# Kernel optimization log

Measured on AMD Instinct MI355X. Metric: run time of the kernel, lower is better.

## Reference

```python
import jax, jax.numpy as jnp
import numpy as np

B, SQ, C = 8, 4096, 1280
CAD = 2048
H, D = 20, 64          # heads x head_dim = hidden_size
NT = 4                 # num IP tokens
TXT = 77               # text tokens
IP_SCALE = 1.0


def setup_inputs() -> dict:
    key = jax.random.key(0)
    ks = jax.random.split(key, 9)
    s = 0.02
    return {
        "hidden_states": jax.random.normal(ks[0], (B, SQ, C), jnp.float32),
        "encoder_hidden_states": jax.random.normal(ks[1], (B, TXT + NT, CAD), jnp.float32),
        "Wq": jax.random.normal(ks[2], (C, C), jnp.float32) * s,
        "Wk": jax.random.normal(ks[3], (CAD, C), jnp.float32) * s,
        "Wv": jax.random.normal(ks[4], (CAD, C), jnp.float32) * s,
        "Wk_ip": jax.random.normal(ks[5], (CAD, C), jnp.float32) * s,
        "Wv_ip": jax.random.normal(ks[6], (CAD, C), jnp.float32) * s,
        "Wo": jax.random.normal(ks[7], (C, C), jnp.float32) * s,
        "bo": jnp.zeros((C,), jnp.float32),
    }


def _heads(x):
    # [b, s, C] -> [b, H, s, D]
    b, s, _ = x.shape
    return x.reshape(b, s, H, D).transpose(0, 2, 1, 3)


def _attend(q, k, v):
    scale = jnp.asarray(1.0 / np.sqrt(D), q.dtype)
    probs = jax.nn.softmax(jnp.einsum('bhqd,bhkd->bhqk', q, k) * scale, axis=-1)
    return jnp.einsum('bhqk,bhkd->bhqd', probs, v)


def reference(hidden_states, encoder_hidden_states, Wq, Wk, Wv, Wk_ip, Wv_ip, Wo, bo):
    residual = hidden_states
    txt = encoder_hidden_states[:, :-NT, :]   # [B, 77, CAD]
    ip = encoder_hidden_states[:, -NT:, :]    # [B, 4, CAD]

    q = _heads(hidden_states @ Wq)            # [B, H, SQ, D]
    k = _heads(txt @ Wk)
    v = _heads(txt @ Wv)
    out = _attend(q, k, v)                    # text branch

    ip_k = _heads(ip @ Wk_ip)
    ip_v = _heads(ip @ Wv_ip)
    out = out + IP_SCALE * _attend(q, ip_k, ip_v)  # IP-adapter branch

    b = out.shape[0]
    out = out.transpose(0, 2, 1, 3).reshape(b, SQ, C)  # merge heads
    out = out @ Wo + bo
    return out + residual
```

## Files before the change

### kernel.cpp

```cpp
#include <hip/hip_runtime.h>
#include <hip/hip_bf16.h>
#include <cstdint>
#include <cstddef>


typedef __bf16 bf16_t;
typedef __bf16 bf16x8 __attribute__((ext_vector_type(8)));
typedef __bf16 bf16x4 __attribute__((ext_vector_type(4)));
typedef float  f32x4  __attribute__((ext_vector_type(4)));
typedef unsigned int u32x4 __attribute__((ext_vector_type(4)));

using as3_void  = __attribute__((address_space(3))) void;
using as1_cvoid = const __attribute__((address_space(1))) void;

#define TXT_ 77

__device__ __forceinline__ bf16x8 ld16(const void* p) {
  u32x4 v = *(const u32x4*)p;
  return __builtin_bit_cast(bf16x8, v);
}

template <int EPI>
__device__ __forceinline__ void gemm256_body(
    char* smem, const bf16_t* __restrict__ A, const bf16_t* __restrict__ Bt,
    void* __restrict__ Cout, int g, int ntn, int N, int K,
    const float* __restrict__ bias, const bf16_t* __restrict__ residual)
{
  const int tid = threadIdx.x, lane = tid & 63, wid = tid >> 6;
  const int wm = wid >> 2, wn = wid & 3;

  const long bm = (long)(g / ntn) * 256;
  const long bn = (long)(g % ntn) * 256;
  const int NTk = K >> 5;

  const int srow = lane >> 2;
  const int scol = ((lane & 3) ^ ((lane >> 3) & 3)) * 8;

  auto stageA = [&](int t) {
    const int buf = t & 3;
    const long k0 = (long)t << 5;
#pragma unroll
    for (int j = 0; j < 2; ++j) {
      const int ci = j * 8 + wid;
      const bf16_t* gp = A + (bm + ci * 16 + srow) * (long)K + k0 + scol;
      __builtin_amdgcn_global_load_lds((as1_cvoid*)gp,
          (as3_void*)(smem + buf * 16384 + ci * 1024), 16, 0, 0);
    }
  };
  auto stageB = [&](int t) {
    const int buf = t & 3;
    const long k0 = (long)t << 5;
#pragma unroll
    for (int j = 0; j < 2; ++j) {
      const int ci = j * 8 + wid;
      const bf16_t* gp = Bt + (bn + ci * 16 + srow) * (long)K + k0 + scol;
      __builtin_amdgcn_global_load_lds((as1_cvoid*)gp,
          (as3_void*)(smem + 65536 + buf * 16384 + ci * 1024), 16, 0, 0);
    }
  };

  const int l15 = lane & 15, kq = lane >> 4;
  const int rc16 = (kq ^ ((l15 >> 1) & 3)) << 4;

  f32x4 acc[8][4] = {};
  bf16x8 afr[4], bfr[4];

  stageA(0); stageB(0); stageA(1); stageB(1);
  asm volatile("s_waitcnt vmcnt(4)" ::: "memory");
  __builtin_amdgcn_s_barrier();

  for (int t = 0; t < NTk; ++t) {
    const char* sa = smem + (t & 3) * 16384;
    const char* sb = smem + 65536 + (t & 3) * 16384;
    const bool pf = (t + 2 < NTk);

#pragma unroll
    for (int n = 0; n < 4; ++n)
      bfr[n] = ld16(sb + (wn * 64 + n * 16 + l15) * 64 + rc16);
#pragma unroll
    for (int m = 0; m < 4; ++m)
      afr[m] = ld16(sa + (wm * 128 + m * 16 + l15) * 64 + rc16);
    if (pf) stageA(t + 2);
    __builtin_amdgcn_s_setprio(1);
#pragma unroll
    for (int m = 0; m < 4; ++m)
#pragma unroll
      for (int n = 0; n < 4; ++n)
        acc[m][n] = __builtin_amdgcn_mfma_f32_16x16x32_bf16(afr[m], bfr[n], acc[m][n], 0, 0, 0);
    __builtin_amdgcn_s_setprio(0);

#pragma unroll
    for (int m = 0; m < 4; ++m)
      afr[m] = ld16(sa + (wm * 128 + (m + 4) * 16 + l15) * 64 + rc16);
    if (pf) stageB(t + 2);
    __builtin_amdgcn_s_setprio(1);
#pragma unroll
    for (int m = 0; m < 4; ++m)
#pragma unroll
      for (int n = 0; n < 4; ++n)
        acc[m + 4][n] = __builtin_amdgcn_mfma_f32_16x16x32_bf16(afr[m], bfr[n], acc[m + 4][n], 0, 0, 0);
    __builtin_amdgcn_s_setprio(0);

    if (t == NTk - 2) asm volatile("s_waitcnt vmcnt(0)" ::: "memory");
    else              asm volatile("s_waitcnt vmcnt(4)" ::: "memory");
    __builtin_amdgcn_s_barrier();
  }

  const int orow0 = (lane >> 4) << 2;
  if constexpr (EPI == 0) {
    bf16_t* cl = (bf16_t*)smem;
    const int lrow0 = wm * 128 + orow0;
    const int lcol0 = wn * 64 + l15;
#pragma unroll
    for (int m = 0; m < 8; ++m)
#pragma unroll
      for (int n = 0; n < 4; ++n)
#pragma unroll
        for (int r = 0; r < 4; ++r)
          cl[(lrow0 + m * 16 + r) * 256 + lcol0 + n * 16] = (bf16_t)acc[m][n][r];
    __syncthreads();
    const int rr = tid >> 5, cc = tid & 31;
#pragma unroll
    for (int s = 0; s < 16; ++s) {
      const int row = s * 16 + rr;
      const u32x4 v = *(const u32x4*)(cl + row * 256 + cc * 8);
      *(u32x4*)((bf16_t*)Cout + (bm + row) * (long)N + bn + cc * 8) = v;
    }
  } else {
#pragma unroll
    for (int m = 0; m < 8; ++m) {
#pragma unroll
      for (int n = 0; n < 4; ++n) {
        const long col = bn + wn * 64 + n * 16 + l15;
#pragma unroll
        for (int r = 0; r < 4; ++r) {
          const long row = bm + wm * 128 + m * 16 + orow0 + r;
          ((float*)Cout)[row * N + col] =
              acc[m][n][r] + bias[col] + (float)residual[row * N + col];
        }
      }
    }
  }
}

__global__ __launch_bounds__(512, 2)
void gemm1_fused(const bf16_t* __restrict__ hsb, const bf16_t* __restrict__ Wq_t,
                 bf16_t* __restrict__ qb,
                 const bf16_t* __restrict__ a_txt, const bf16_t* __restrict__ Wkv_t,
                 bf16_t* __restrict__ kv_txt,
                 const bf16_t* __restrict__ a_ip, const bf16_t* __restrict__ Wip_t,
                 bf16_t* __restrict__ kv_ip)
{
  __shared__ __align__(16) char smem[131072];
  const int bid = blockIdx.x;
  const bf16_t *A, *Bt;
  bf16_t* C;
  int g, ntn, N, K;
  if (bid < 640) {
    g = (bid & 7) * 80 + (bid >> 3);
    A = hsb; Bt = Wq_t; C = qb; ntn = 5; N = 1280; K = 1280;
  } else if (bid < 670) {
    g = bid - 640; A = a_txt; Bt = Wkv_t; C = kv_txt; ntn = 10; N = 2560; K = 2048;
  } else {
    g = bid - 670; A = a_ip; Bt = Wip_t; C = kv_ip; ntn = 10; N = 2560; K = 2048;
  }
  gemm256_body<0>(smem, A, Bt, C, g, ntn, N, K, nullptr, nullptr);
}

__global__ __launch_bounds__(512, 2)
void gemm2(const bf16_t* __restrict__ A, const bf16_t* __restrict__ Bt,
           float* __restrict__ Cout, const float* __restrict__ bias,
           const bf16_t* __restrict__ residual)
{
  __shared__ __align__(16) char smem[131072];
  const int bid = blockIdx.x;
  const int g = (bid & 7) * 80 + (bid >> 3);
  gemm256_body<2>(smem, A, Bt, Cout, g, 5, 1280, 1280, bias, residual);
}

__global__ __launch_bounds__(256, 3)
void attn_fused(const bf16_t* __restrict__ q, const bf16_t* __restrict__ kvt,
                const bf16_t* __restrict__ kvip, bf16_t* __restrict__ outp)
{
  __shared__ __align__(16) bf16_t K_lds[80 * 64];
  __shared__ __align__(16) bf16_t Kip_lds[16 * 64];
  __shared__ __align__(16) bf16_t Vt_lds[64 * 128];
  __shared__ __align__(16) bf16_t P_lds[4][16 * 128];

  const int tid = threadIdx.x, lane = tid & 63, wid = tid >> 6;
  const int h = blockIdx.y, b = blockIdx.z;
  const int kvcol = h << 6;

  for (int idx = tid; idx < 640; idx += 256) {
    const int j = idx >> 3, c = idx & 7;
    bf16x8 v = {};
    if (j < TXT_) v = ld16(kvt + (long)(b * 80 + j) * 2560 + kvcol + c * 8);
    *(bf16x8*)((char*)K_lds + j * 128 + ((c ^ (j & 7)) << 4)) = v;
  }
  if (tid < 128) {
    const int j = tid >> 3, c = tid & 7;
    bf16x8 v = {};
    if (j < 4) v = ld16(kvip + (long)(b * 4 + j) * 2560 + kvcol + c * 8);
    *(bf16x8*)((char*)Kip_lds + j * 128 + ((c ^ (j & 7)) << 4)) = v;
  }
  for (int idx = tid; idx < 1024; idx += 256) {
    const int key = idx >> 3, c = idx & 7;
    bf16x8 v = {};
    if (key < TXT_)
      v = ld16(kvt + (long)(b * 80 + key) * 2560 + 1280 + kvcol + c * 8);
    else if (key >= 96 && key < 100)
      v = ld16(kvip + (long)(b * 4 + key - 96) * 2560 + 1280 + kvcol + c * 8);
#pragma unroll
    for (int e = 0; e < 8; ++e) {
      const int d = c * 8 + e;
      *(bf16_t*)((char*)Vt_lds + d * 256 + ((key * 2) ^ ((d & 7) << 4))) = v[e];
    }
  }
  for (int idx = tid; idx < 1024; idx += 256)
    *(bf16x8*)((char*)P_lds + idx * 16) = (bf16x8){};
  __syncthreads();

  const int l15 = lane & 15, hi = lane >> 4;
  const int dblk = hi << 3;
  const int prow0 = hi << 2;
  const float scale = 0.125f;
  char* const pw = (char*)P_lds[wid];

  const long qrow0 = (long)b * 4096 + ((long)blockIdx.x << 8) + (wid << 6);
  bf16x8 qf[4][2];
#pragma unroll
  for (int ms = 0; ms < 4; ++ms) {
    const bf16_t* qp = q + (qrow0 + ms * 16 + l15) * 1280 + kvcol;
    qf[ms][0] = ld16(qp + dblk);
    qf[ms][1] = ld16(qp + 32 + dblk);
  }

#pragma unroll
  for (int ms = 0; ms < 4; ++ms) {
    f32x4 sc[5];
#pragma unroll
    for (int t = 0; t < 5; ++t) {
      const int j = (t << 4) + l15;
      const bf16x8 k0 = ld16((char*)K_lds + j * 128 + ((hi ^ (j & 7)) << 4));
      const bf16x8 k1 = ld16((char*)K_lds + j * 128 + (((4 + hi) ^ (j & 7)) << 4));
      f32x4 z = {0.f, 0.f, 0.f, 0.f};
      z = __builtin_amdgcn_mfma_f32_16x16x32_bf16(qf[ms][0], k0, z, 0, 0, 0);
      z = __builtin_amdgcn_mfma_f32_16x16x32_bf16(qf[ms][1], k1, z, 0, 0, 0);
      sc[t] = z;
    }
#pragma unroll
    for (int t = 0; t < 5; ++t) {
      const bool valid = ((t << 4) + l15) < TXT_;
#pragma unroll
      for (int r = 0; r < 4; ++r)
        sc[t][r] = valid ? sc[t][r] * scale : -1e30f;
    }

#pragma unroll
    for (int r = 0; r < 4; ++r) {
      float m = sc[0][r];
#pragma unroll
      for (int t = 1; t < 5; ++t) m = fmaxf(m, sc[t][r]);
      m = fmaxf(m, __shfl_xor(m, 1));
      m = fmaxf(m, __shfl_xor(m, 2));
      m = fmaxf(m, __shfl_xor(m, 4));
      m = fmaxf(m, __shfl_xor(m, 8));
      float l = 0.f;
#pragma unroll
      for (int t = 0; t < 5; ++t) { const float p = __expf(sc[t][r] - m); sc[t][r] = p; l += p; }
      l += __shfl_xor(l, 1);
      l += __shfl_xor(l, 2);
      l += __shfl_xor(l, 4);
      l += __shfl_xor(l, 8);
      const float inv = 1.f / l;
      const int row = prow0 + r;
#pragma unroll
      for (int t = 0; t < 5; ++t)
        *(bf16_t*)(pw + row * 256 + ((((t << 4) + l15) * 2) ^ ((row & 7) << 4))) =
            (bf16_t)(sc[t][r] * inv);
    }

    {
      const bf16x8 ki0 = ld16((char*)Kip_lds + l15 * 128 + ((hi ^ (l15 & 7)) << 4));
      const bf16x8 ki1 = ld16((char*)Kip_lds + l15 * 128 + (((4 + hi) ^ (l15 & 7)) << 4));
      f32x4 z = {0.f, 0.f, 0.f, 0.f};
      z = __builtin_amdgcn_mfma_f32_16x16x32_bf16(qf[ms][0], ki0, z, 0, 0, 0);
      z = __builtin_amdgcn_mfma_f32_16x16x32_bf16(qf[ms][1], ki1, z, 0, 0, 0);
      const bool vip = l15 < 4;
#pragma unroll
      for (int r = 0; r < 4; ++r) {
        const float s = vip ? z[r] * scale : -1e30f;
        float m = s;
        m = fmaxf(m, __shfl_xor(m, 1));
        m = fmaxf(m, __shfl_xor(m, 2));
        m = fmaxf(m, __shfl_xor(m, 4));
        m = fmaxf(m, __shfl_xor(m, 8));
        const float p = __expf(s - m);
        float l = p;
        l += __shfl_xor(l, 1);
        l += __shfl_xor(l, 2);
        l += __shfl_xor(l, 4);
        l += __shfl_xor(l, 8);
        const int row = prow0 + r;
        *(bf16_t*)(pw + row * 256 + (((96 + l15) * 2) ^ ((row & 7) << 4))) =
            (bf16_t)(p * (1.f / l));
      }
    }

    f32x4 o[4] = {};
#pragma unroll
    for (int s = 0; s < 4; ++s) {
      const bf16x8 pa =
          ld16(pw + l15 * 256 + ((((s << 2) + hi) << 4) ^ ((l15 & 7) << 4)));
#pragma unroll
      for (int n = 0; n < 4; ++n) {
        const int d = (n << 4) + l15;
        const bf16x8 vb =
            ld16((char*)Vt_lds + d * 256 + ((((s << 2) + hi) << 4) ^ ((d & 7) << 4)));
        o[n] = __builtin_amdgcn_mfma_f32_16x16x32_bf16(pa, vb, o[n], 0, 0, 0);
      }
    }

    const long orow = qrow0 + ms * 16 + prow0;
#pragma unroll
    for (int n = 0; n < 4; ++n)
#pragma unroll
      for (int r = 0; r < 4; ++r)
        outp[(orow + r) * 1280 + kvcol + (n << 4) + l15] = (bf16_t)o[n][r];
  }
}

__global__ __launch_bounds__(256)
void prep(const float* __restrict__ hs, bf16_t* __restrict__ hsb,
          const float* __restrict__ Wq, const float* __restrict__ Wo,
          const float* __restrict__ Wk, const float* __restrict__ Wv,
          const float* __restrict__ Wki, const float* __restrict__ Wvi,
          bf16_t* __restrict__ Wq_t, bf16_t* __restrict__ Wo_t,
          bf16_t* __restrict__ Wkv_t, bf16_t* __restrict__ Wip_t,
          const float* __restrict__ enc, bf16_t* __restrict__ a_txt,
          bf16_t* __restrict__ a_ip)
{
  __shared__ float tile[32][33];
  const int bid = blockIdx.x, tid = threadIdx.x;

  if (bid < 40960) {
    const long i = ((long)bid * 256 + tid) * 4;
    const float4 v = *(const float4*)(hs + i);
    bf16x4 r;
    r[0] = (bf16_t)v.x; r[1] = (bf16_t)v.y; r[2] = (bf16_t)v.z; r[3] = (bf16_t)v.w;
    *(bf16x4*)(hsb + i) = r;
  } else if (bid < 56320) {
    const int idx = bid - 40960;
    const int z = idx / 2560, rem = idx % 2560;
    const int kx = rem & 63, ny = rem >> 6;
    const float* in;
    bf16_t* out;
    int K;
    switch (z) {
      case 0:  in = Wq;  out = Wq_t;                      K = 1280; break;
      case 1:  in = Wo;  out = Wo_t;                      K = 1280; break;
      case 2:  in = Wk;  out = Wkv_t;                     K = 2048; break;
      case 3:  in = Wv;  out = Wkv_t + (long)1280 * 2048; K = 2048; break;
      case 4:  in = Wki; out = Wip_t;                     K = 2048; break;
      default: in = Wvi; out = Wip_t + (long)1280 * 2048; K = 2048; break;
    }
    const int k0 = kx * 32, n0 = ny * 32;
    if (k0 < K) {
      const int tx = tid & 31, ty = tid >> 5;
      for (int i = ty; i < 32; i += 8)
        tile[i][tx] = in[(long)(k0 + i) * 1280 + n0 + tx];
      __syncthreads();
      for (int i = ty; i < 32; i += 8)
        out[(long)(n0 + i) * K + k0 + tx] = (bf16_t)tile[tx][i];
    }
  } else {
    const long t4 = ((long)(bid - 56320) * 256 + tid) * 4;
    const long NTXT = 768L * 2048;
    bf16x4 r;
    r[0] = r[1] = r[2] = r[3] = (bf16_t)0.f;
    if (t4 < NTXT) {
      const int row = (int)(t4 >> 11), col = (int)(t4 & 2047);
      if (row < 640) {
        const int b = row / 80, j = row - b * 80;
        if (j < TXT_) {
          const float4 v = *(const float4*)(enc + (((long)(b * 81 + j)) << 11) + col);
          r[0] = (bf16_t)v.x; r[1] = (bf16_t)v.y; r[2] = (bf16_t)v.z; r[3] = (bf16_t)v.w;
        }
      }
      *(bf16x4*)(a_txt + t4) = r;
    } else {
      const long u = t4 - NTXT;
      const int row = (int)(u >> 11), col = (int)(u & 2047);
      if (row < 32) {
        const int b = row >> 2, j = row & 3;
        const float4 v = *(const float4*)(enc + (((long)(b * 81 + TXT_ + j)) << 11) + col);
        r[0] = (bf16_t)v.x; r[1] = (bf16_t)v.y; r[2] = (bf16_t)v.z; r[3] = (bf16_t)v.w;
      }
      *(bf16x4*)(a_ip + u) = r;
    }
  }
}

extern "C" void kernel_launch(void* const* d_in, const int* in_sizes, int n_in,
                              void* d_out, int out_size, void* d_ws, size_t ws_size,
                              hipStream_t stream)
{
  (void)in_sizes; (void)n_in; (void)out_size; (void)ws_size;
  const float* hs  = (const float*)d_in[0];
  const float* enc = (const float*)d_in[1];
  const float* Wq  = (const float*)d_in[2];
  const float* Wk  = (const float*)d_in[3];
  const float* Wv  = (const float*)d_in[4];
  const float* Wki = (const float*)d_in[5];
  const float* Wvi = (const float*)d_in[6];
  const float* Wo  = (const float*)d_in[7];
  const float* bo  = (const float*)d_in[8];

  char* ws = (char*)d_ws;
  size_t off = 0;
  auto alloc = [&](size_t bytes) {
    char* p = ws + off;
    off += (bytes + 255) & ~(size_t)255;
    return p;
  };
  bf16_t* buf1   = (bf16_t*)alloc(83886080);
  bf16_t* qb     = (bf16_t*)alloc(83886080);
  bf16_t* Wq_t   = (bf16_t*)alloc(3276800);
  bf16_t* Wo_t   = (bf16_t*)alloc(3276800);
  bf16_t* Wkv_t  = (bf16_t*)alloc(10485760);
  bf16_t* Wip_t  = (bf16_t*)alloc(10485760);
  bf16_t* a_txt  = (bf16_t*)alloc(3145728);
  bf16_t* a_ip   = (bf16_t*)alloc(1048576);
  bf16_t* kv_txt = (bf16_t*)alloc(3932160);
  bf16_t* kv_ip  = (bf16_t*)alloc(1310720);

  prep<<<58368, 256, 0, stream>>>(hs, buf1, Wq, Wo, Wk, Wv, Wki, Wvi,
                                  Wq_t, Wo_t, Wkv_t, Wip_t, enc, a_txt, a_ip);

  gemm1_fused<<<680, 512, 0, stream>>>(buf1, Wq_t, qb,
                                       a_txt, Wkv_t, kv_txt,
                                       a_ip, Wip_t, kv_ip);

  attn_fused<<<dim3(16, 20, 8), 256, 0, stream>>>(qb, kv_txt, kv_ip, qb);

  gemm2<<<640, 512, 0, stream>>>(qb, Wo_t, (float*)d_out, bo, buf1);
}
```

Baseline: 421.9 us.

## Load GEMM B fragments directly to registers, halve LDS footprint

The B operand is no longer staged through LDS. Each wave loads its B fragments straight from global memory into registers, double-buffered two k-steps ahead, and the loop is unrolled by two to alternate between the buffers. This halves shared memory to 64KB, so the bf16 epilogue is split into two halves to fit the staging buffer. It removes LDS traffic and LDS capacity pressure for B, at the cost of redundant global/L2 reads of B across waves and more registers.

```diff
diff --git a/kernel.cpp b/kernel.cpp
--- a/kernel.cpp
+++ b/kernel.cpp
@@ -47,36 +47,31 @@
           (as3_void*)(smem + buf * 16384 + ci * 1024), 16, 0, 0);
     }
   };
-  auto stageB = [&](int t) {
-    const int buf = t & 3;
-    const long k0 = (long)t << 5;
-#pragma unroll
-    for (int j = 0; j < 2; ++j) {
-      const int ci = j * 8 + wid;
-      const bf16_t* gp = Bt + (bn + ci * 16 + srow) * (long)K + k0 + scol;
-      __builtin_amdgcn_global_load_lds((as1_cvoid*)gp,
-          (as3_void*)(smem + 65536 + buf * 16384 + ci * 1024), 16, 0, 0);
-    }
-  };
 
   const int l15 = lane & 15, kq = lane >> 4;
   const int rc16 = (kq ^ ((l15 >> 1) & 3)) << 4;
 
+  const bf16_t* bbase = Bt + (bn + wn * 64 + l15) * (long)K + kq * 8;
+
+  auto loadB = [&](int t, bf16x8 (&bq)[4]) {
+    const long k0 = (long)t << 5;
+#pragma unroll
+    for (int n = 0; n < 4; ++n)
+      bq[n] = ld16(bbase + (long)n * 16 * K + k0);
+  };
+
   f32x4 acc[8][4] = {};
-  bf16x8 afr[4], bfr[4];
-
-  stageA(0); stageB(0); stageA(1); stageB(1);
+  bf16x8 bA[4], bB[4];
+
+  stageA(0); stageA(1);
+  loadB(0, bA); loadB(1, bB);
   asm volatile("s_waitcnt vmcnt(4)" ::: "memory");
   __builtin_amdgcn_s_barrier();
 
-  for (int t = 0; t < NTk; ++t) {
+  auto iter = [&](int t, bf16x8 (&bcur)[4]) {
     const char* sa = smem + (t & 3) * 16384;
-    const char* sb = smem + 65536 + (t & 3) * 16384;
     const bool pf = (t + 2 < NTk);
-
-#pragma unroll
-    for (int n = 0; n < 4; ++n)
-      bfr[n] = ld16(sb + (wn * 64 + n * 16 + l15) * 64 + rc16);
+    bf16x8 afr[4];
 #pragma unroll
     for (int m = 0; m < 4; ++m)
       afr[m] = ld16(sa + (wm * 128 + m * 16 + l15) * 64 + rc16);
@@ -86,45 +81,53 @@
     for (int m = 0; m < 4; ++m)
 #pragma unroll
       for (int n = 0; n < 4; ++n)
-        acc[m][n] = __builtin_amdgcn_mfma_f32_16x16x32_bf16(afr[m], bfr[n], acc[m][n], 0, 0, 0);
+        acc[m][n] = __builtin_amdgcn_mfma_f32_16x16x32_bf16(afr[m], bcur[n], acc[m][n], 0, 0, 0);
     __builtin_amdgcn_s_setprio(0);
-
 #pragma unroll
     for (int m = 0; m < 4; ++m)
       afr[m] = ld16(sa + (wm * 128 + (m + 4) * 16 + l15) * 64 + rc16);
-    if (pf) stageB(t + 2);
     __builtin_amdgcn_s_setprio(1);
 #pragma unroll
     for (int m = 0; m < 4; ++m)
 #pragma unroll
       for (int n = 0; n < 4; ++n)
-        acc[m + 4][n] = __builtin_amdgcn_mfma_f32_16x16x32_bf16(afr[m], bfr[n], acc[m + 4][n], 0, 0, 0);
+        acc[m + 4][n] = __builtin_amdgcn_mfma_f32_16x16x32_bf16(afr[m], bcur[n], acc[m + 4][n], 0, 0, 0);
     __builtin_amdgcn_s_setprio(0);
-
-    if (t == NTk - 2) asm volatile("s_waitcnt vmcnt(0)" ::: "memory");
-    else              asm volatile("s_waitcnt vmcnt(4)" ::: "memory");
+    if (pf) loadB(t + 2, bcur);
+    if (t == NTk - 2)      asm volatile("s_waitcnt vmcnt(0)" ::: "memory");
+    else if (t < NTk - 1)  asm volatile("s_waitcnt vmcnt(6)" ::: "memory");
     __builtin_amdgcn_s_barrier();
+  };
+
+  for (int t = 0; t < NTk; t += 2) {
+    iter(t, bA);
+    iter(t + 1, bB);
   }
 
   const int orow0 = (lane >> 4) << 2;
   if constexpr (EPI == 0) {
     bf16_t* cl = (bf16_t*)smem;
-    const int lrow0 = wm * 128 + orow0;
-    const int lcol0 = wn * 64 + l15;
-#pragma unroll
-    for (int m = 0; m < 8; ++m)
-#pragma unroll
-      for (int n = 0; n < 4; ++n)
-#pragma unroll
-        for (int r = 0; r < 4; ++r)
-          cl[(lrow0 + m * 16 + r) * 256 + lcol0 + n * 16] = (bf16_t)acc[m][n][r];
-    __syncthreads();
     const int rr = tid >> 5, cc = tid & 31;
 #pragma unroll
-    for (int s = 0; s < 16; ++s) {
-      const int row = s * 16 + rr;
-      const u32x4 v = *(const u32x4*)(cl + row * 256 + cc * 8);
-      *(u32x4*)((bf16_t*)Cout + (bm + row) * (long)N + bn + cc * 8) = v;
+    for (int h = 0; h < 2; ++h) {
+      __syncthreads();
+      if (wm == h) {
+#pragma unroll
+        for (int m = 0; m < 8; ++m)
+#pragma unroll
+          for (int n = 0; n < 4; ++n)
+#pragma unroll
+            for (int r = 0; r < 4; ++r)
+              cl[(m * 16 + orow0 + r) * 256 + wn * 64 + n * 16 + l15] =
+                  (bf16_t)acc[m][n][r];
+      }
+      __syncthreads();
+#pragma unroll
+      for (int s = 0; s < 8; ++s) {
+        const int row = s * 16 + rr;
+        const u32x4 v = *(const u32x4*)(cl + row * 256 + cc * 8);
+        *(u32x4*)((bf16_t*)Cout + (bm + h * 128 + row) * (long)N + bn + cc * 8) = v;
+      }
     }
   } else {
 #pragma unroll
@@ -151,7 +154,7 @@
                  const bf16_t* __restrict__ a_ip, const bf16_t* __restrict__ Wip_t,
                  bf16_t* __restrict__ kv_ip)
 {
-  __shared__ __align__(16) char smem[131072];
+  __shared__ __align__(16) char smem[65536];
   const int bid = blockIdx.x;
   const bf16_t *A, *Bt;
   bf16_t* C;
@@ -172,7 +175,7 @@
            float* __restrict__ Cout, const float* __restrict__ bias,
            const bf16_t* __restrict__ residual)
 {
-  __shared__ __align__(16) char smem[131072];
+  __shared__ __align__(16) char smem[65536];
   const int bid = blockIdx.x;
   const int g = (bid & 7) * 80 + (bid >> 3);
   gemm256_body<2>(smem, A, Bt, Cout, g, 5, 1280, 1280, bias, residual);
```

New measurement: 548.3 us. 1.3x slower.
